# Performance work log

Hardware: AMD Instinct MI355X
Metric: run time of the kernel (lower is better)

The kernel has to match this reference:

```python
import jax, jax.numpy as jnp
import numpy as np

NH = 32          # num_attention_heads
LAYER_ID = 3     # per-layer scaling coeff = LAYER_ID + 1
SQ, B, H = 1024, 2, 4096
MEM_LEN = 1024
HD = H // NH


def setup_inputs() -> dict:
    key = jax.random.key(0)
    ks = jax.random.split(key, 6)
    hidden_states = jax.random.normal(ks[0], (SQ, B, H), dtype=jnp.float32)
    mem = jax.random.normal(ks[1], (B, MEM_LEN, 2 * NH * HD), dtype=jnp.float32) * 0.5
    qkv_w = jax.random.normal(ks[2], (3 * H, H), dtype=jnp.float32) * 0.02
    qkv_b = jax.random.normal(ks[3], (3 * H,), dtype=jnp.float32) * 0.02
    dense_w = jax.random.normal(ks[4], (H, H), dtype=jnp.float32) * 0.02
    dense_b = jax.random.normal(ks[5], (H,), dtype=jnp.float32) * 0.02
    # causal mask over new tokens; mem positions fully visible. True = masked.
    kv = MEM_LEN + SQ
    mask = ((jnp.arange(kv)[None, :] - MEM_LEN) > jnp.arange(SQ)[:, None])
    mask = mask[None, None, :, :]  # [1,1,sq,kv]
    # position ids of new tokens continue after the mem cache: [b, sq]
    position_ids = jnp.broadcast_to(MEM_LEN + jnp.arange(SQ, dtype=jnp.int64), (B, SQ))
    return {"hidden_states": hidden_states, "mask": mask, "position_ids": position_ids,
            "mem": mem, "qkv_w": qkv_w, "qkv_b": qkv_b, "dense_w": dense_w, "dense_b": dense_b}


def _rotate_half(x):
    x1, x2 = jnp.split(x, 2, axis=-1)
    return jnp.concatenate((-x2, x1), axis=-1)


def _rotary_tables(max_pos):
    inv_freq = 1.0 / (10000.0 ** (jnp.arange(0, HD, 2, dtype=jnp.float32) / HD))
    t = jnp.arange(max_pos, dtype=jnp.float32)
    freqs = jnp.einsum('i,j->ij', t, inv_freq)          # [L, HD/2]
    emb = jnp.concatenate((freqs, freqs), axis=-1)      # [L, HD]
    return jnp.cos(emb), jnp.sin(emb)


def reference(hidden_states, mask, position_ids, mem, qkv_w, qkv_b, dense_w, dense_b):
    sq, b, h = hidden_states.shape
    coeff = float(LAYER_ID + 1)
    # QKV projection: [sq,b,3H] -> [sq,b,nh,3*hd] -> split
    mixed = jnp.einsum('sbh,oh->sbo', hidden_states, qkv_w) + qkv_b
    mixed = mixed.reshape(sq, b, NH, 3 * HD)
    q, k, v = jnp.split(mixed, 3, axis=-1)              # each [sq,b,nh,hd]
    # rotary embedding with position indices (position_ids: [b,sq] -> [sq,b])
    pos = position_ids.T                                 # [sq,b]
    cos_t, sin_t = _rotary_tables(MEM_LEN + SQ)          # table up to max pos + 1
    cos = cos_t[pos][:, :, None, :]                      # [sq,b,1,hd]
    sin = sin_t[pos][:, :, None, :]
    q = q * cos + _rotate_half(q) * sin
    k = k * cos + _rotate_half(k) * sin
    # mem-KV concat: mem [b, mem_len, 2*nh*hd] -> memk/memv [mem_len,b,nh,hd]
    m = mem.reshape(b, MEM_LEN, 2, NH, HD).transpose(2, 1, 0, 3, 4)
    k = jnp.concatenate((m[0], k), axis=0)               # [kv,b,nh,hd]
    v = jnp.concatenate((m[1], v), axis=0)
    # per-layer scaled attention scores
    q = q / (np.sqrt(HD) * coeff)
    scores = jnp.einsum('sbnh,tbnh->bnst', q, k)         # [b,nh,sq,kv]
    scores = jnp.where(mask, -10000.0, scores)
    scores = scores * coeff
    probs = jax.nn.softmax(scores, axis=-1)
    ctx = jnp.einsum('bnst,tbnh->sbnh', probs, v).reshape(sq, b, h)
    out = jnp.einsum('sbh,oh->sbo', ctx, dense_w) + dense_b
    return out
```

## Files before the change

kernel.cpp:

```cpp
#include <hip/hip_runtime.h>


typedef __attribute__((ext_vector_type(4))) float f32x4;
typedef __attribute__((ext_vector_type(8))) short bf16x8;
typedef unsigned short u16;

#define SQ   1024
#define BSZ  2
#define H    4096
#define NH   32
#define HD   128
#define MEML 1024
#define KV   2048

__device__ __forceinline__ u16 f32_to_bf16(float f) {
  union { float f; unsigned int u; } v; v.f = f;
  unsigned int r = v.u + 0x7FFFu + ((v.u >> 16) & 1u);
  return (u16)(r >> 16);
}
__device__ __forceinline__ float bf16_to_f32(u16 x) {
  union { unsigned int u; float f; } v; v.u = ((unsigned int)x) << 16; return v.f;
}

__device__ __forceinline__ void gload_lds16(const void* g, void* l) {
  __builtin_amdgcn_global_load_lds((const __attribute__((address_space(1))) void*)g,
                                   (__attribute__((address_space(3))) void*)l, 16, 0, 0);
}

__global__ __launch_bounds__(256) void conv_bf16(const float* __restrict__ in,
                                                 u16* __restrict__ out, int n4) {
  int idx = blockIdx.x * 256 + threadIdx.x;
  if (idx < n4) {
    float4 v = ((const float4*)in)[idx];
    ushort4 o;
    o.x = f32_to_bf16(v.x); o.y = f32_to_bf16(v.y);
    o.z = f32_to_bf16(v.z); o.w = f32_to_bf16(v.w);
    ((ushort4*)out)[idx] = o;
  }
}

__global__ __launch_bounds__(256) void rope_tables(float* __restrict__ cost, float* __restrict__ sint) {
  int idx = blockIdx.x * 256 + threadIdx.x;
  int s = idx >> 6, j = idx & 63;
  float inv = powf(10000.0f, -(float)j / 64.0f);
  float ang = (float)(MEML + s) * inv;
  cost[idx] = cosf(ang);
  sint[idx] = sinf(ang);
}

template <typename OUT_T, int NF>
__global__ __launch_bounds__(512, 2) void gemmT(const u16* __restrict__ A, const u16* __restrict__ B,
                                                const float* __restrict__ bias, OUT_T* __restrict__ C,
                                                int N, int K) {
  constexpr int WN = NF * 16;
  constexpr int NH0 = (NF + 1) / 2;
  constexpr int SB2 = NF - (NF >> 1);
  __shared__ char lds[2][32768 + NF * 8192];
  const int tid = threadIdx.x;
  const int lane = tid & 63;
  const int w = tid >> 6;
  const int wm = w >> 2, wn = w & 3;
  const int rl = lane & 15, cg = lane >> 4;
  const int m0 = blockIdx.y * 256, n0 = blockIdx.x * (NF * 64);
  const int nt = K >> 6;

  const int srow = tid >> 3;
  const int scb = ((tid & 7) << 4) ^ ((srow & 7) << 4);

  auto stage_a = [&](int tile, int ua) {
    if (tile >= nt) return;
    gload_lds16((const char*)(A + (size_t)(m0 + ua * 64 + srow) * K + (size_t)tile * 64) + scb,
                lds[tile & 1] + ua * 8192 + tid * 16);
  };
  auto stage_b = [&](int tile, int ub) {
    if (tile >= nt) return;
    gload_lds16((const char*)(B + (size_t)(n0 + ub * 64 + srow) * K + (size_t)tile * 64) + scb,
                lds[tile & 1] + 32768 + ub * 8192 + tid * 16);
  };

  f32x4 acc[8][NF];
#pragma unroll
  for (int i = 0; i < 8; ++i)
#pragma unroll
    for (int j = 0; j < NF; ++j) acc[i][j] = (f32x4){0.f, 0.f, 0.f, 0.f};

  bf16x8 af[4][2], bf[NF][2];

  auto read_a = [&](const char* buf, int mh) {
#pragma unroll
    for (int mi = 0; mi < 4; ++mi) {
      int R = wm * 128 + mh * 64 + mi * 16 + rl;
#pragma unroll
      for (int kk = 0; kk < 2; ++kk) {
        int cb = (kk * 64 + cg * 16) ^ ((R & 7) << 4);
        af[mi][kk] = *(const bf16x8*)(buf + R * 128 + cb);
      }
    }
  };
  auto read_b1 = [&](const char* buf, int nl) {
    int R = wn * WN + nl * 16 + rl;
#pragma unroll
    for (int kk = 0; kk < 2; ++kk) {
      int cb = (kk * 64 + cg * 16) ^ ((R & 7) << 4);
      bf[nl][kk] = *(const bf16x8*)(buf + 32768 + R * 128 + cb);
    }
  };
  auto mfset = [&](int mh, int lo, int hi) {
    __builtin_amdgcn_s_setprio(1);
#pragma unroll
    for (int kk = 0; kk < 2; ++kk)
#pragma unroll
      for (int mi = 0; mi < 4; ++mi)
#pragma unroll
        for (int nl = 0; nl < NF; ++nl)
          if (nl >= lo && nl < hi)
            acc[mh * 4 + mi][nl] = __builtin_amdgcn_mfma_f32_16x16x32_bf16(
                af[mi][kk], bf[nl][kk], acc[mh * 4 + mi][nl], 0, 0, 0);
    __builtin_amdgcn_s_setprio(0);
  };

#pragma unroll
  for (int ua = 0; ua < 4; ++ua) stage_a(0, ua);
#pragma unroll
  for (int ub = 0; ub < NF; ++ub) stage_b(0, ub);
#pragma unroll
  for (int ub = 0; ub < NF; ++ub) stage_b(1, ub);
  if (NF == 2)      { asm volatile("s_waitcnt vmcnt(2)" ::: "memory"); }
  else if (NF == 3) { asm volatile("s_waitcnt vmcnt(3)" ::: "memory"); }
  else              { asm volatile("s_waitcnt vmcnt(4)" ::: "memory"); }
  __builtin_amdgcn_s_barrier();

  for (int kt = 0; kt < nt; ++kt) {
    const char* buf = lds[kt & 1];
    read_a(buf, 0);
#pragma unroll
    for (int nl = 0; nl < NH0; ++nl) read_b1(buf, nl);
    stage_a(kt + 1, 0); stage_a(kt + 1, 1);
    __builtin_amdgcn_s_barrier();
    asm volatile("s_waitcnt lgkmcnt(0)" ::: "memory");
    mfset(0, 0, NH0);
    __builtin_amdgcn_s_barrier();
#pragma unroll
    for (int nl = NH0; nl < NF; ++nl) read_b1(buf, nl);
    stage_a(kt + 1, 2); stage_a(kt + 1, 3);
    __builtin_amdgcn_s_barrier();
    asm volatile("s_waitcnt lgkmcnt(0)" ::: "memory");
    mfset(0, NH0, NF);
    __builtin_amdgcn_s_barrier();
    read_a(buf, 1);
#pragma unroll
    for (int ub = 0; ub < SB2; ++ub) stage_b(kt + 2, ub);
    __builtin_amdgcn_s_barrier();
    asm volatile("s_waitcnt lgkmcnt(0)" ::: "memory");
    mfset(1, NH0, NF);
    __builtin_amdgcn_s_barrier();
#pragma unroll
    for (int ub = SB2; ub < NF; ++ub) stage_b(kt + 2, ub);
    __builtin_amdgcn_s_barrier();
    mfset(1, 0, NH0);
    if (kt + 2 < nt) {
      if (NF == 2)      { asm volatile("s_waitcnt vmcnt(2)" ::: "memory"); }
      else if (NF == 3) { asm volatile("s_waitcnt vmcnt(3)" ::: "memory"); }
      else              { asm volatile("s_waitcnt vmcnt(4)" ::: "memory"); }
    } else if (kt + 1 < nt) {
      asm volatile("s_waitcnt vmcnt(0)" ::: "memory");
    }
    __builtin_amdgcn_s_barrier();
  }

#pragma unroll
  for (int ni = 0; ni < NF; ++ni) {
    int col = n0 + wn * WN + ni * 16 + rl;
    float bv = bias[col];
#pragma unroll
    for (int mi = 0; mi < 8; ++mi) {
      int rbase = m0 + wm * 128 + mi * 16 + cg * 4;
#pragma unroll
      for (int j = 0; j < 4; ++j) {
        float v = acc[mi][ni][j] + bv;
        if constexpr (sizeof(OUT_T) == 2)
          C[(size_t)(rbase + j) * N + col] = (OUT_T)f32_to_bf16(v);
        else
          C[(size_t)(rbase + j) * N + col] = (OUT_T)v;
      }
    }
  }
}

__global__ __launch_bounds__(256) void prep_qk(const u16* __restrict__ mixed,
                                               const float* __restrict__ cost,
                                               const float* __restrict__ sint,
                                               u16* __restrict__ Qb, u16* __restrict__ Kb) {
  int s0 = blockIdx.x * 64, head = blockIdx.y;
  int b = head >> 5, nh = head & 31;
  int tid = threadIdx.x;
  const float qs = 0.08838834764831845f;
#pragma unroll
  for (int i = 0; i < 16; ++i) {
    int flat = i * 256 + tid;
    int sl = flat >> 6, j = flat & 63;
    int s = s0 + sl;
    size_t base = ((size_t)(s * 2 + b)) * 12288 + (size_t)nh * 384;
    float q1 = bf16_to_f32(mixed[base + j]),       q2 = bf16_to_f32(mixed[base + j + 64]);
    float k1 = bf16_to_f32(mixed[base + 128 + j]), k2 = bf16_to_f32(mixed[base + 192 + j]);
    float c = cost[s * 64 + j], sn = sint[s * 64 + j];
    float q1r = q1 * c - q2 * sn, q2r = q2 * c + q1 * sn;
    float k1r = k1 * c - k2 * sn, k2r = k2 * c + k1 * sn;
    size_t qoff = ((size_t)head * SQ + s) * HD;
    Qb[qoff + j]      = f32_to_bf16(q1r * qs);
    Qb[qoff + j + 64] = f32_to_bf16(q2r * qs);
    size_t koff = ((size_t)head * KV + MEML + s) * HD;
    Kb[koff + j]      = f32_to_bf16(k1r);
    Kb[koff + j + 64] = f32_to_bf16(k2r);
  }
}

__global__ __launch_bounds__(256) void prep_kv(const u16* __restrict__ mixed,
                                               const float* __restrict__ mem,
                                               u16* __restrict__ Kb, u16* __restrict__ Vtb) {
  int t0 = blockIdx.x * 64, head = blockIdx.y;
  int b = head >> 5, nh = head & 31;
  __shared__ u16 vt[128 * 72];
  int tid = threadIdx.x;
  if (t0 < MEML) {
#pragma unroll
    for (int i = 0; i < 32; ++i) {
      int flat = i * 256 + tid;
      int tl = flat >> 7, d = flat & 127;
      float kvv = mem[((size_t)b * MEML + t0 + tl) * 8192 + (size_t)nh * HD + d];
      Kb[((size_t)head * KV + t0 + tl) * HD + d] = f32_to_bf16(kvv);
    }
  }
#pragma unroll
  for (int i = 0; i < 32; ++i) {
    int flat = i * 256 + tid;
    int tl = flat >> 7, d = flat & 127;
    int t = t0 + tl;
    u16 v;
    if (t < MEML) v = f32_to_bf16(mem[((size_t)b * MEML + t) * 8192 + 4096 + (size_t)nh * HD + d]);
    else          v = mixed[((size_t)((t - MEML) * 2 + b)) * 12288 + (size_t)nh * 384 + 256 + d];
    vt[d * 72 + tl] = v;
  }
  __syncthreads();
#pragma unroll
  for (int i = 0; i < 4; ++i) {
    int c = i * 256 + tid;
    int d = c >> 3, slot = c & 7;
    *(bf16x8*)(Vtb + ((size_t)head * HD + d) * KV + t0 + slot * 8) =
        *(const bf16x8*)(vt + d * 72 + slot * 8);
  }
}

__global__ __launch_bounds__(512) void attn_fwd(const u16* __restrict__ Qb, const u16* __restrict__ Kb,
                                                const u16* __restrict__ Vtb, u16* __restrict__ ctx) {
  __shared__ u16 Ks[2][64 * 128];
  __shared__ u16 Vts[2][128 * 64];
  __shared__ u16 Ps[8 * 16 * 64];
  const int tid = threadIdx.x;
  const int lane = tid & 63;
  const int w = tid >> 6;
  const int q0 = blockIdx.x * 128;
  const int head = blockIdx.y;
  const int rl = lane & 15, cg = lane >> 4;

  bf16x8 qf[4];
  {
    const u16* Qrow = Qb + ((size_t)head * SQ + q0 + w * 16 + rl) * HD;
#pragma unroll
    for (int kk = 0; kk < 4; ++kk)
      qf[kk] = *(const bf16x8*)(Qrow + kk * 32 + cg * 8);
  }

  f32x4 acc[8];
#pragma unroll
  for (int i = 0; i < 8; ++i) acc[i] = (f32x4){0.f, 0.f, 0.f, 0.f};
  float mrow[4] = {-3.0e38f, -3.0e38f, -3.0e38f, -3.0e38f};
  float lrow[4] = {0.f, 0.f, 0.f, 0.f};

  const int ntile = (MEML + q0 + 128) >> 6;

  auto stageKV = [&](int it) {
    int t0 = it * 64;
    int buf = it & 1;
#pragma unroll
    for (int i = 0; i < 2; ++i) {
      int flat = i * 512 + tid;
      int row = flat >> 4;
      int scb = ((flat & 15) << 4) ^ ((row & 7) << 4);
      gload_lds16((const char*)(Kb + ((size_t)head * KV + t0 + row) * HD) + scb,
                  (char*)Ks[buf] + (flat << 4));
    }
#pragma unroll
    for (int i = 0; i < 2; ++i) {
      int flat = i * 512 + tid;
      int row = flat >> 3;
      int scb = ((flat & 7) << 4) ^ ((row & 7) << 4);
      gload_lds16((const char*)(Vtb + ((size_t)head * HD + row) * KV + t0) + scb,
                  (char*)Vts[buf] + (flat << 4));
    }
  };

  stageKV(0);

  for (int it = 0; it < ntile; ++it) {
    const int t0 = it * 64;
    if (it + 1 < ntile) {
      stageKV(it + 1);
      asm volatile("s_waitcnt vmcnt(4)" ::: "memory");
    } else {
      asm volatile("s_waitcnt vmcnt(0)" ::: "memory");
    }
    __builtin_amdgcn_s_barrier();
    const char* Kbuf = (const char*)Ks[it & 1];
    const char* Vbuf = (const char*)Vts[it & 1];
    const bool live = (t0 - MEML) <= (q0 + w * 16 + 15);
    if (live) {
      f32x4 sf[4];
#pragma unroll
      for (int tn = 0; tn < 4; ++tn) {
        f32x4 s = (f32x4){0.f, 0.f, 0.f, 0.f};
#pragma unroll
        for (int kk = 0; kk < 4; ++kk) {
          int row = tn * 16 + rl;
          int cb = (kk * 64 + cg * 16) ^ ((row & 7) << 4);
          bf16x8 kf = *(const bf16x8*)(Kbuf + row * 256 + cb);
          s = __builtin_amdgcn_mfma_f32_16x16x32_bf16(qf[kk], kf, s, 0, 0, 0);
        }
        sf[tn] = s;
      }
      if (t0 + 63 > MEML + q0 + w * 16) {
#pragma unroll
        for (int tn = 0; tn < 4; ++tn)
#pragma unroll
          for (int j = 0; j < 4; ++j) {
            int t = t0 + tn * 16 + rl;
            int srow = q0 + w * 16 + cg * 4 + j;
            if (t - MEML > srow) sf[tn][j] = -40000.0f;
          }
      }
      float mt[4];
#pragma unroll
      for (int j = 0; j < 4; ++j)
        mt[j] = fmaxf(fmaxf(sf[0][j], sf[1][j]), fmaxf(sf[2][j], sf[3][j]));
#pragma unroll
      for (int off = 1; off <= 8; off <<= 1)
#pragma unroll
        for (int j = 0; j < 4; ++j) mt[j] = fmaxf(mt[j], __shfl_xor(mt[j], off, 64));
      float pscale[4];
#pragma unroll
      for (int j = 0; j < 4; ++j) {
        float mn = fmaxf(mrow[j], mt[j]);
        pscale[j] = __expf(mrow[j] - mn);
        mrow[j] = mn;
      }
      float lsum[4] = {0.f, 0.f, 0.f, 0.f};
#pragma unroll
      for (int tn = 0; tn < 4; ++tn)
#pragma unroll
        for (int j = 0; j < 4; ++j) {
          float p = __expf(sf[tn][j] - mrow[j]);
          lsum[j] += p;
          int prow = cg * 4 + j;
          int colb = (tn * 16 + rl) * 2;
          int addr = w * 2048 + prow * 128 + (colb ^ ((prow & 7) << 4));
          *(u16*)((char*)Ps + addr) = f32_to_bf16(p);
        }
#pragma unroll
      for (int off = 1; off <= 8; off <<= 1)
#pragma unroll
        for (int j = 0; j < 4; ++j) lsum[j] += __shfl_xor(lsum[j], off, 64);
#pragma unroll
      for (int j = 0; j < 4; ++j) lrow[j] = lrow[j] * pscale[j] + lsum[j];
#pragma unroll
      for (int dn = 0; dn < 8; ++dn)
#pragma unroll
        for (int j = 0; j < 4; ++j) acc[dn][j] *= pscale[j];
#pragma unroll
      for (int dn = 0; dn < 8; ++dn) {
#pragma unroll
        for (int kk2 = 0; kk2 < 2; ++kk2) {
          int pcb = (kk2 * 64 + cg * 16) ^ ((rl & 7) << 4);
          bf16x8 pf = *(const bf16x8*)((const char*)Ps + w * 2048 + rl * 128 + pcb);
          int vrow = dn * 16 + rl;
          int vcb = (kk2 * 64 + cg * 16) ^ ((vrow & 7) << 4);
          bf16x8 vf = *(const bf16x8*)(Vbuf + vrow * 128 + vcb);
          acc[dn] = __builtin_amdgcn_mfma_f32_16x16x32_bf16(pf, vf, acc[dn], 0, 0, 0);
        }
      }
    }
    __builtin_amdgcn_s_barrier();
  }

  const int b = head >> 5, nh = head & 31;
#pragma unroll
  for (int dn = 0; dn < 8; ++dn)
#pragma unroll
    for (int j = 0; j < 4; ++j) {
      int srow = q0 + w * 16 + cg * 4 + j;
      float v = acc[dn][j] / lrow[j];
      ctx[((size_t)(srow * 2 + b)) * H + (size_t)nh * HD + dn * 16 + rl] = f32_to_bf16(v);
    }
}

extern "C" void kernel_launch(void* const* d_in, const int* in_sizes, int n_in,
                              void* d_out, int out_size, void* d_ws, size_t ws_size,
                              hipStream_t stream) {
  const float* hidden  = (const float*)d_in[0];
  const float* mem     = (const float*)d_in[3];
  const float* qkv_w   = (const float*)d_in[4];
  const float* qkv_b   = (const float*)d_in[5];
  const float* dense_w = (const float*)d_in[6];
  const float* dense_b = (const float*)d_in[7];
  float* out = (float*)d_out;
  char* ws = (char*)d_ws;

  u16* mixed = (u16*)ws;
  char* R1 = ws + 100663296;
  u16* hid_bf = (u16*)R1;
  u16* qw_bf  = (u16*)(R1 + 16777216);
  u16* Qb  = (u16*)R1;
  u16* Kb  = (u16*)(R1 + 16777216);
  u16* Vtb = (u16*)(R1 + 50331648);
  u16* ctx = (u16*)(R1 + 83886080);
  u16* dw_bf = (u16*)(R1 + 100663296);
  float* cost = (float*)(ws + 234881024);
  float* sint = (float*)(ws + 234881024 + 262144);

  conv_bf16<<<8192, 256, 0, stream>>>(hidden, hid_bf, 2097152);
  conv_bf16<<<49152, 256, 0, stream>>>(qkv_w, qw_bf, 12582912);
  rope_tables<<<256, 256, 0, stream>>>(cost, sint);
  gemmT<u16, 3><<<dim3(64, 8), 512, 0, stream>>>(hid_bf, qw_bf, qkv_b, mixed, 12288, 4096);
  prep_qk<<<dim3(16, 64), 256, 0, stream>>>(mixed, cost, sint, Qb, Kb);
  prep_kv<<<dim3(32, 64), 256, 0, stream>>>(mixed, mem, Kb, Vtb);
  conv_bf16<<<16384, 256, 0, stream>>>(dense_w, dw_bf, 4194304);
  attn_fwd<<<dim3(8, 64), 512, 0, stream>>>(Qb, Kb, Vtb, ctx);
  gemmT<float, 2><<<dim3(32, 8), 512, 0, stream>>>(ctx, dw_bf, dense_b, out, 4096, 4096);
}
```

Baseline: 563.0 us.

## Specialize GEMMs with double A-fragment registers, fewer barriers, and XCD-aware block swizzle

Replaces the templated GEMM with two specialized kernels for the QKV and dense projections. Each holds both halves of the A fragments in registers at once, so the MFMA phases are reordered and some barrier and LDS-read stages are dropped. It also remaps workgroup IDs with a stride-8 swizzle so neighbouring tiles land on the same XCD and share L2. The extra fragment registers raise register pressure, and the reordered staging could change how well global loads overlap with compute.

Measured after the change: 574.6 us. 2.1% more time.

```diff
diff --git a/kernel.cpp b/kernel.cpp
--- a/kernel.cpp
+++ b/kernel.cpp
@@ -48,20 +48,19 @@
   sint[idx] = sinf(ang);
 }
 
-template <typename OUT_T, int NF>
-__global__ __launch_bounds__(512, 2) void gemmT(const u16* __restrict__ A, const u16* __restrict__ B,
-                                                const float* __restrict__ bias, OUT_T* __restrict__ C,
-                                                int N, int K) {
-  constexpr int WN = NF * 16;
-  constexpr int NH0 = (NF + 1) / 2;
-  constexpr int SB2 = NF - (NF >> 1);
-  __shared__ char lds[2][32768 + NF * 8192];
+__global__ __launch_bounds__(512, 2) void gemm3p(const u16* __restrict__ A, const u16* __restrict__ B,
+                                                 const float* __restrict__ bias, u16* __restrict__ C,
+                                                 int N, int K) {
+  __shared__ char lds[2][57344];
   const int tid = threadIdx.x;
   const int lane = tid & 63;
   const int w = tid >> 6;
   const int wm = w >> 2, wn = w & 3;
   const int rl = lane & 15, cg = lane >> 4;
-  const int m0 = blockIdx.y * 256, n0 = blockIdx.x * (NF * 64);
+  const int nwg = gridDim.x * gridDim.y;
+  const int lid = blockIdx.y * gridDim.x + blockIdx.x;
+  const int swz = (lid & 7) * (nwg >> 3) + (lid >> 3);
+  const int m0 = (swz / gridDim.x) * 256, n0 = (swz % gridDim.x) * 192;
   const int nt = K >> 6;
 
   const int srow = tid >> 3;
@@ -78,111 +77,215 @@
                 lds[tile & 1] + 32768 + ub * 8192 + tid * 16);
   };
 
-  f32x4 acc[8][NF];
+  f32x4 acc[8][3];
 #pragma unroll
   for (int i = 0; i < 8; ++i)
 #pragma unroll
-    for (int j = 0; j < NF; ++j) acc[i][j] = (f32x4){0.f, 0.f, 0.f, 0.f};
-
-  bf16x8 af[4][2], bf[NF][2];
-
-  auto read_a = [&](const char* buf, int mh) {
+    for (int j = 0; j < 3; ++j) acc[i][j] = (f32x4){0.f, 0.f, 0.f, 0.f};
+
+  bf16x8 af0[4][2], af1[4][2], bf[3][2];
+
+  auto read_am = [&](const char* buf, int mh, bf16x8 (&dst)[4][2]) {
 #pragma unroll
     for (int mi = 0; mi < 4; ++mi) {
       int R = wm * 128 + mh * 64 + mi * 16 + rl;
 #pragma unroll
       for (int kk = 0; kk < 2; ++kk) {
         int cb = (kk * 64 + cg * 16) ^ ((R & 7) << 4);
-        af[mi][kk] = *(const bf16x8*)(buf + R * 128 + cb);
+        dst[mi][kk] = *(const bf16x8*)(buf + R * 128 + cb);
       }
     }
   };
   auto read_b1 = [&](const char* buf, int nl) {
-    int R = wn * WN + nl * 16 + rl;
+    int R = wn * 48 + nl * 16 + rl;
 #pragma unroll
     for (int kk = 0; kk < 2; ++kk) {
       int cb = (kk * 64 + cg * 16) ^ ((R & 7) << 4);
       bf[nl][kk] = *(const bf16x8*)(buf + 32768 + R * 128 + cb);
     }
   };
-  auto mfset = [&](int mh, int lo, int hi) {
-    __builtin_amdgcn_s_setprio(1);
-#pragma unroll
-    for (int kk = 0; kk < 2; ++kk)
-#pragma unroll
-      for (int mi = 0; mi < 4; ++mi)
-#pragma unroll
-        for (int nl = 0; nl < NF; ++nl)
-          if (nl >= lo && nl < hi)
-            acc[mh * 4 + mi][nl] = __builtin_amdgcn_mfma_f32_16x16x32_bf16(
-                af[mi][kk], bf[nl][kk], acc[mh * 4 + mi][nl], 0, 0, 0);
-    __builtin_amdgcn_s_setprio(0);
-  };
-
-#pragma unroll
-  for (int ua = 0; ua < 4; ++ua) stage_a(0, ua);
-#pragma unroll
-  for (int ub = 0; ub < NF; ++ub) stage_b(0, ub);
-#pragma unroll
-  for (int ub = 0; ub < NF; ++ub) stage_b(1, ub);
-  if (NF == 2)      { asm volatile("s_waitcnt vmcnt(2)" ::: "memory"); }
-  else if (NF == 3) { asm volatile("s_waitcnt vmcnt(3)" ::: "memory"); }
-  else              { asm volatile("s_waitcnt vmcnt(4)" ::: "memory"); }
+
+#pragma unroll
+  for (int u = 0; u < 4; ++u) stage_a(0, u);
+#pragma unroll
+  for (int u = 0; u < 3; ++u) stage_b(0, u);
+#pragma unroll
+  for (int u = 0; u < 3; ++u) stage_b(1, u);
+  asm volatile("s_waitcnt vmcnt(3)" ::: "memory");
   __builtin_amdgcn_s_barrier();
 
   for (int kt = 0; kt < nt; ++kt) {
     const char* buf = lds[kt & 1];
-    read_a(buf, 0);
-#pragma unroll
-    for (int nl = 0; nl < NH0; ++nl) read_b1(buf, nl);
+    read_am(buf, 0, af0);
+    read_b1(buf, 0); read_b1(buf, 1);
     stage_a(kt + 1, 0); stage_a(kt + 1, 1);
     __builtin_amdgcn_s_barrier();
     asm volatile("s_waitcnt lgkmcnt(0)" ::: "memory");
-    mfset(0, 0, NH0);
-    __builtin_amdgcn_s_barrier();
-#pragma unroll
-    for (int nl = NH0; nl < NF; ++nl) read_b1(buf, nl);
+    __builtin_amdgcn_s_setprio(1);
+#pragma unroll
+    for (int kk = 0; kk < 2; ++kk)
+#pragma unroll
+      for (int mi = 0; mi < 4; ++mi) {
+        acc[mi][0] = __builtin_amdgcn_mfma_f32_16x16x32_bf16(af0[mi][kk], bf[0][kk], acc[mi][0], 0, 0, 0);
+        acc[mi][1] = __builtin_amdgcn_mfma_f32_16x16x32_bf16(af0[mi][kk], bf[1][kk], acc[mi][1], 0, 0, 0);
+      }
+    __builtin_amdgcn_s_setprio(0);
+    __builtin_amdgcn_s_barrier();
+    read_am(buf, 1, af1);
+    read_b1(buf, 2);
     stage_a(kt + 1, 2); stage_a(kt + 1, 3);
     __builtin_amdgcn_s_barrier();
     asm volatile("s_waitcnt lgkmcnt(0)" ::: "memory");
-    mfset(0, NH0, NF);
-    __builtin_amdgcn_s_barrier();
-    read_a(buf, 1);
-#pragma unroll
-    for (int ub = 0; ub < SB2; ++ub) stage_b(kt + 2, ub);
-    __builtin_amdgcn_s_barrier();
-    asm volatile("s_waitcnt lgkmcnt(0)" ::: "memory");
-    mfset(1, NH0, NF);
-    __builtin_amdgcn_s_barrier();
-#pragma unroll
-    for (int ub = SB2; ub < NF; ++ub) stage_b(kt + 2, ub);
-    __builtin_amdgcn_s_barrier();
-    mfset(1, 0, NH0);
-    if (kt + 2 < nt) {
-      if (NF == 2)      { asm volatile("s_waitcnt vmcnt(2)" ::: "memory"); }
-      else if (NF == 3) { asm volatile("s_waitcnt vmcnt(3)" ::: "memory"); }
-      else              { asm volatile("s_waitcnt vmcnt(4)" ::: "memory"); }
-    } else if (kt + 1 < nt) {
-      asm volatile("s_waitcnt vmcnt(0)" ::: "memory");
-    }
-    __builtin_amdgcn_s_barrier();
-  }
-
-#pragma unroll
-  for (int ni = 0; ni < NF; ++ni) {
-    int col = n0 + wn * WN + ni * 16 + rl;
+    __builtin_amdgcn_s_setprio(1);
+#pragma unroll
+    for (int kk = 0; kk < 2; ++kk)
+#pragma unroll
+      for (int mi = 0; mi < 4; ++mi) {
+        acc[4 + mi][1] = __builtin_amdgcn_mfma_f32_16x16x32_bf16(af1[mi][kk], bf[1][kk], acc[4 + mi][1], 0, 0, 0);
+        acc[4 + mi][2] = __builtin_amdgcn_mfma_f32_16x16x32_bf16(af1[mi][kk], bf[2][kk], acc[4 + mi][2], 0, 0, 0);
+      }
+    __builtin_amdgcn_s_setprio(0);
+    __builtin_amdgcn_s_barrier();
+    stage_b(kt + 2, 0); stage_b(kt + 2, 1); stage_b(kt + 2, 2);
+    __builtin_amdgcn_s_barrier();
+    __builtin_amdgcn_s_setprio(1);
+#pragma unroll
+    for (int kk = 0; kk < 2; ++kk)
+#pragma unroll
+      for (int mi = 0; mi < 4; ++mi) {
+        acc[mi][2] = __builtin_amdgcn_mfma_f32_16x16x32_bf16(af0[mi][kk], bf[2][kk], acc[mi][2], 0, 0, 0);
+        acc[4 + mi][0] = __builtin_amdgcn_mfma_f32_16x16x32_bf16(af1[mi][kk], bf[0][kk], acc[4 + mi][0], 0, 0, 0);
+      }
+    __builtin_amdgcn_s_setprio(0);
+    if (kt + 2 < nt)      { asm volatile("s_waitcnt vmcnt(3)" ::: "memory"); }
+    else if (kt + 1 < nt) { asm volatile("s_waitcnt vmcnt(0)" ::: "memory"); }
+    __builtin_amdgcn_s_barrier();
+  }
+
+#pragma unroll
+  for (int ni = 0; ni < 3; ++ni) {
+    int col = n0 + wn * 48 + ni * 16 + rl;
     float bv = bias[col];
 #pragma unroll
     for (int mi = 0; mi < 8; ++mi) {
       int rbase = m0 + wm * 128 + mi * 16 + cg * 4;
 #pragma unroll
-      for (int j = 0; j < 4; ++j) {
-        float v = acc[mi][ni][j] + bv;
-        if constexpr (sizeof(OUT_T) == 2)
-          C[(size_t)(rbase + j) * N + col] = (OUT_T)f32_to_bf16(v);
-        else
-          C[(size_t)(rbase + j) * N + col] = (OUT_T)v;
-      }
+      for (int j = 0; j < 4; ++j)
+        C[(size_t)(rbase + j) * N + col] = f32_to_bf16(acc[mi][ni][j] + bv);
+    }
+  }
+}
+
+__global__ __launch_bounds__(512, 2) void gemm2p(const u16* __restrict__ A, const u16* __restrict__ B,
+                                                 const float* __restrict__ bias, float* __restrict__ C,
+                                                 int N, int K) {
+  __shared__ char lds[2][49152];
+  const int tid = threadIdx.x;
+  const int lane = tid & 63;
+  const int w = tid >> 6;
+  const int wm = w >> 2, wn = w & 3;
+  const int rl = lane & 15, cg = lane >> 4;
+  const int nwg = gridDim.x * gridDim.y;
+  const int lid = blockIdx.y * gridDim.x + blockIdx.x;
+  const int swz = (lid & 7) * (nwg >> 3) + (lid >> 3);
+  const int m0 = (swz / gridDim.x) * 256, n0 = (swz % gridDim.x) * 128;
+  const int nt = K >> 6;
+
+  const int srow = tid >> 3;
+  const int scb = ((tid & 7) << 4) ^ ((srow & 7) << 4);
+
+  auto stage_a = [&](int tile, int ua) {
+    if (tile >= nt) return;
+    gload_lds16((const char*)(A + (size_t)(m0 + ua * 64 + srow) * K + (size_t)tile * 64) + scb,
+                lds[tile & 1] + ua * 8192 + tid * 16);
+  };
+  auto stage_b = [&](int tile, int ub) {
+    if (tile >= nt) return;
+    gload_lds16((const char*)(B + (size_t)(n0 + ub * 64 + srow) * K + (size_t)tile * 64) + scb,
+                lds[tile & 1] + 32768 + ub * 8192 + tid * 16);
+  };
+
+  f32x4 acc[8][2];
+#pragma unroll
+  for (int i = 0; i < 8; ++i)
+#pragma unroll
+    for (int j = 0; j < 2; ++j) acc[i][j] = (f32x4){0.f, 0.f, 0.f, 0.f};
+
+  bf16x8 af0[4][2], af1[4][2], bf[2][2];
+
+  auto read_am = [&](const char* buf, int mh, bf16x8 (&dst)[4][2]) {
+#pragma unroll
+    for (int mi = 0; mi < 4; ++mi) {
+      int R = wm * 128 + mh * 64 + mi * 16 + rl;
+#pragma unroll
+      for (int kk = 0; kk < 2; ++kk) {
+        int cb = (kk * 64 + cg * 16) ^ ((R & 7) << 4);
+        dst[mi][kk] = *(const bf16x8*)(buf + R * 128 + cb);
+      }
+    }
+  };
+  auto read_b1 = [&](const char* buf, int nl) {
+    int R = wn * 32 + nl * 16 + rl;
+#pragma unroll
+    for (int kk = 0; kk < 2; ++kk) {
+      int cb = (kk * 64 + cg * 16) ^ ((R & 7) << 4);
+      bf[nl][kk] = *(const bf16x8*)(buf + 32768 + R * 128 + cb);
+    }
+  };
+
+#pragma unroll
+  for (int u = 0; u < 4; ++u) stage_a(0, u);
+  stage_b(0, 0); stage_b(0, 1);
+  stage_b(1, 0); stage_b(1, 1);
+  asm volatile("s_waitcnt vmcnt(2)" ::: "memory");
+  __builtin_amdgcn_s_barrier();
+
+  for (int kt = 0; kt < nt; ++kt) {
+    const char* buf = lds[kt & 1];
+    read_am(buf, 0, af0);
+    read_b1(buf, 0); read_b1(buf, 1);
+    stage_a(kt + 1, 0); stage_a(kt + 1, 1);
+    __builtin_amdgcn_s_barrier();
+    asm volatile("s_waitcnt lgkmcnt(0)" ::: "memory");
+    __builtin_amdgcn_s_setprio(1);
+#pragma unroll
+    for (int kk = 0; kk < 2; ++kk)
+#pragma unroll
+      for (int mi = 0; mi < 4; ++mi) {
+        acc[mi][0] = __builtin_amdgcn_mfma_f32_16x16x32_bf16(af0[mi][kk], bf[0][kk], acc[mi][0], 0, 0, 0);
+        acc[mi][1] = __builtin_amdgcn_mfma_f32_16x16x32_bf16(af0[mi][kk], bf[1][kk], acc[mi][1], 0, 0, 0);
+      }
+    __builtin_amdgcn_s_setprio(0);
+    __builtin_amdgcn_s_barrier();
+    read_am(buf, 1, af1);
+    stage_a(kt + 1, 2); stage_a(kt + 1, 3);
+    stage_b(kt + 2, 0); stage_b(kt + 2, 1);
+    __builtin_amdgcn_s_barrier();
+    asm volatile("s_waitcnt lgkmcnt(0)" ::: "memory");
+    __builtin_amdgcn_s_setprio(1);
+#pragma unroll
+    for (int kk = 0; kk < 2; ++kk)
+#pragma unroll
+      for (int mi = 0; mi < 4; ++mi) {
+        acc[4 + mi][0] = __builtin_amdgcn_mfma_f32_16x16x32_bf16(af1[mi][kk], bf[0][kk], acc[4 + mi][0], 0, 0, 0);
+        acc[4 + mi][1] = __builtin_amdgcn_mfma_f32_16x16x32_bf16(af1[mi][kk], bf[1][kk], acc[4 + mi][1], 0, 0, 0);
+      }
+    __builtin_amdgcn_s_setprio(0);
+    if (kt + 2 < nt)      { asm volatile("s_waitcnt vmcnt(2)" ::: "memory"); }
+    else if (kt + 1 < nt) { asm volatile("s_waitcnt vmcnt(0)" ::: "memory"); }
+    __builtin_amdgcn_s_barrier();
+  }
+
+#pragma unroll
+  for (int ni = 0; ni < 2; ++ni) {
+    int col = n0 + wn * 32 + ni * 16 + rl;
+    float bv = bias[col];
+#pragma unroll
+    for (int mi = 0; mi < 8; ++mi) {
+      int rbase = m0 + wm * 128 + mi * 16 + cg * 4;
+#pragma unroll
+      for (int j = 0; j < 4; ++j)
+        C[(size_t)(rbase + j) * N + col] = acc[mi][ni][j] + bv;
     }
   }
 }
@@ -334,8 +437,8 @@
 #pragma unroll
           for (int j = 0; j < 4; ++j) {
             int t = t0 + tn * 16 + rl;
-            int srow = q0 + w * 16 + cg * 4 + j;
-            if (t - MEML > srow) sf[tn][j] = -40000.0f;
+            int srowq = q0 + w * 16 + cg * 4 + j;
+            if (t - MEML > srowq) sf[tn][j] = -40000.0f;
           }
       }
       float mt[4];
@@ -396,9 +499,9 @@
   for (int dn = 0; dn < 8; ++dn)
 #pragma unroll
     for (int j = 0; j < 4; ++j) {
-      int srow = q0 + w * 16 + cg * 4 + j;
+      int srowq = q0 + w * 16 + cg * 4 + j;
       float v = acc[dn][j] / lrow[j];
-      ctx[((size_t)(srow * 2 + b)) * H + (size_t)nh * HD + dn * 16 + rl] = f32_to_bf16(v);
+      ctx[((size_t)(srowq * 2 + b)) * H + (size_t)nh * HD + dn * 16 + rl] = f32_to_bf16(v);
     }
 }
 
@@ -429,10 +532,10 @@
   conv_bf16<<<8192, 256, 0, stream>>>(hidden, hid_bf, 2097152);
   conv_bf16<<<49152, 256, 0, stream>>>(qkv_w, qw_bf, 12582912);
   rope_tables<<<256, 256, 0, stream>>>(cost, sint);
-  gemmT<u16, 3><<<dim3(64, 8), 512, 0, stream>>>(hid_bf, qw_bf, qkv_b, mixed, 12288, 4096);
+  gemm3p<<<dim3(64, 8), 512, 0, stream>>>(hid_bf, qw_bf, qkv_b, mixed, 12288, 4096);
   prep_qk<<<dim3(16, 64), 256, 0, stream>>>(mixed, cost, sint, Qb, Kb);
   prep_kv<<<dim3(32, 64), 256, 0, stream>>>(mixed, mem, Kb, Vtb);
   conv_bf16<<<16384, 256, 0, stream>>>(dense_w, dw_bf, 4194304);
   attn_fwd<<<dim3(8, 64), 512, 0, stream>>>(Qb, Kb, Vtb, ctx);
-  gemmT<float, 2><<<dim3(32, 8), 512, 0, stream>>>(ctx, dw_bf, dense_b, out, 4096, 4096);
-}
+  gemm2p<<<dim3(32, 8), 512, 0, stream>>>(ctx, dw_bf, dense_b, out, 4096, 4096);
+}
```
